# Performance work log

Measured on AMD Instinct MI355X. Metric: run time of the kernel, lower is better.

The kernel has to match this reference:

```python
import jax, jax.numpy as jnp
import numpy as np

N = 100000   # nodes
E = 1000000  # edges
G = 64       # graphs in batch
DIN, DH, DOUT = 128, 128, 64
BN_EPS = 1e-5


def setup_inputs() -> dict:
    key = jax.random.key(0)
    ks = jax.random.split(key, 20)
    inp = {}
    inp['x'] = jax.random.normal(ks[0], (N, DIN), dtype=jnp.float32)
    inp['edge_index'] = jax.random.randint(ks[1], (2, E), 0, N, dtype=jnp.int64)
    inp['batch'] = jnp.sort(jax.random.randint(ks[2], (N,), 0, G, dtype=jnp.int64))
    # GCN conv weights (stored [in, out]) + biases
    s = lambda k, i, o: jax.random.normal(k, (i, o), dtype=jnp.float32) / np.sqrt(i)
    inp['W1'] = s(ks[3], DIN, DH);  inp['b1'] = jnp.zeros((DH,), jnp.float32)
    inp['W2'] = s(ks[4], DH, DH);   inp['b2'] = jnp.zeros((DH,), jnp.float32)
    inp['W3'] = s(ks[5], DH, DOUT); inp['b3'] = jnp.zeros((DOUT,), jnp.float32)
    # BatchNorm params/buffers (eval mode)
    inp['g1'] = jnp.ones((DH,), jnp.float32);  inp['beta1'] = jnp.zeros((DH,), jnp.float32)
    inp['g2'] = jnp.ones((DH,), jnp.float32);  inp['beta2'] = jnp.zeros((DH,), jnp.float32)
    inp['mean1'] = jnp.zeros((DH,), jnp.float32); inp['var1'] = jnp.ones((DH,), jnp.float32)
    inp['mean2'] = jnp.zeros((DH,), jnp.float32); inp['var2'] = jnp.ones((DH,), jnp.float32)
    # GlobalAttention gate_nn: Linear(DOUT,DH) ReLU Linear(DH,1)
    inp['Wg1'] = s(ks[6], DOUT, DH); inp['bg1'] = jnp.zeros((DH,), jnp.float32)
    inp['Wg2'] = s(ks[7], DH, 1);    inp['bg2'] = jnp.zeros((1,), jnp.float32)
    # head MLP: Linear(DOUT,DH) ReLU Linear(DH,DOUT)
    inp['Wm1'] = s(ks[8], DOUT, DH); inp['bm1'] = jnp.zeros((DH,), jnp.float32)
    inp['Wm2'] = s(ks[9], DH, DOUT); inp['bm2'] = jnp.zeros((DOUT,), jnp.float32)
    return inp


def _gcn_conv(x, W, b, src, dst):
    # PyG GCNConv: add self-loops, sym-normalize, linear, scatter-sum, bias
    h = x @ W                                            # [N, out]
    deg = jnp.ones((N,), h.dtype).at[dst].add(1.0)       # in-degree + self-loop
    dinv = jax.lax.rsqrt(deg)
    norm = dinv[src] * dinv[dst]                         # [E]
    msg = h[src] * norm[:, None]                         # gather + scale
    out = jax.ops.segment_sum(msg, dst, num_segments=N)  # scatter
    out = out + h * (dinv * dinv)[:, None]               # self-loop term
    return out + b


def _bn(x, g, beta, mean, var):
    return (x - mean) * jax.lax.rsqrt(var + BN_EPS) * g + beta


def reference(x, edge_index, batch, W1, b1, W2, b2, W3, b3,
              g1, beta1, g2, beta2, mean1, var1, mean2, var2,
              Wg1, bg1, Wg2, bg2, Wm1, bm1, Wm2, bm2):
    src, dst = edge_index[0], edge_index[1]
    h = jax.nn.relu(_bn(_gcn_conv(x, W1, b1, src, dst), g1, beta1, mean1, var1))
    h = jax.nn.relu(_bn(_gcn_conv(h, W2, b2, src, dst), g2, beta2, mean2, var2))
    h = _gcn_conv(h, W3, b3, src, dst)                   # [N, DOUT]
    # GlobalAttention pooling: per-graph softmax of gate scores
    gate = jax.nn.relu(h @ Wg1 + bg1) @ Wg2 + bg2        # [N, 1]
    gate = gate[:, 0]
    m = jax.ops.segment_max(gate, batch, num_segments=G)
    e = jnp.exp(gate - m[batch])
    s = jax.ops.segment_sum(e, batch, num_segments=G)
    a = e / s[batch]                                     # [N]
    pooled = jax.ops.segment_sum(h * a[:, None], batch, num_segments=G)  # [G, DOUT]
    # MLP head (dropout off in eval)
    return jax.nn.relu(pooled @ Wm1 + bm1) @ Wm2 + bm2   # [G, DOUT]
```

## Files before the change

kernel.cpp:

```cpp
#include <hip/hip_runtime.h>
#include <hip/hip_bf16.h>
#include <hip/hip_fp16.h>
#include <math.h>

#define NN 100000
#define EE 1000000
#define GG 64
#define BN_EPS 1e-5f
#define CPB 16
#define EB 4096
#define NBLK ((EE + EB - 1) / EB)
#define NBUCK ((NN + 511) / 512)

typedef __attribute__((ext_vector_type(8))) short bf16x8;
typedef __attribute__((ext_vector_type(4))) float f32x4;

__device__ inline short f2bf(float f) {
  unsigned u = __float_as_uint(f);
  u = u + 0x7fff + ((u >> 16) & 1);
  return (short)(u >> 16);
}
__device__ inline float bf2f(short h) {
  return __uint_as_float(((unsigned)(unsigned short)h) << 16);
}

__device__ inline unsigned fenc(float f) {
  int b = __float_as_int(f);
  return (b < 0) ? ~(unsigned)b : ((unsigned)b | 0x80000000u);
}
__device__ inline float fdec(unsigned u) {
  int b = (u & 0x80000000u) ? (int)(u & 0x7fffffffu) : (int)~u;
  return __int_as_float(b);
}

__device__ inline void acc2(float& a0, float& a1, unsigned u) {
  asm("v_fma_mix_f32 %0, %2, 1.0, %0 op_sel:[0,0,0] op_sel_hi:[1,0,0]\n\t"
      "v_fma_mix_f32 %1, %2, 1.0, %1 op_sel:[1,0,0] op_sel_hi:[1,0,0]"
      : "+v"(a0), "+v"(a1)
      : "v"(u));
}
__device__ inline void acc8(float* a, uint4 u) {
  acc2(a[0], a[1], u.x);
  acc2(a[2], a[3], u.y);
  acc2(a[4], a[5], u.z);
  acc2(a[6], a[7], u.w);
}
__device__ inline uint4 zsel(uint4 u, int ok) {
  uint4 r;
  r.x = ok ? u.x : 0u;
  r.y = ok ? u.y : 0u;
  r.z = ok ? u.z : 0u;
  r.w = ok ? u.w : 0u;
  return r;
}

__global__ __launch_bounds__(256) void k_bhist(const int* __restrict__ dst,
                                               int* __restrict__ bhist, int E) {
  __shared__ int h[256];
  int t = threadIdx.x;
  h[t] = 0;
  __syncthreads();
  int base = blockIdx.x * EB;
#pragma unroll
  for (int j = 0; j < EB / 256; ++j) {
    int i = base + j * 256 + t;
    if (i < E) atomicAdd(&h[dst[i] >> 9], 1);
  }
  __syncthreads();
  bhist[blockIdx.x * 256 + t] = h[t];
}

__global__ __launch_bounds__(256) void k_bscan1(int* __restrict__ bhist,
                                                int* __restrict__ btot) {
  __shared__ int s[256];
  int bin = blockIdx.x, t = threadIdx.x;
  int v = (t < NBLK) ? bhist[t * 256 + bin] : 0;
  s[t] = v;
  __syncthreads();
  for (int o = 1; o < 256; o <<= 1) {
    int u = (t >= o) ? s[t - o] : 0;
    __syncthreads();
    s[t] += u;
    __syncthreads();
  }
  if (t < NBLK) bhist[t * 256 + bin] = s[t] - v;
  if (t == 255) btot[bin] = s[255];
}

__global__ __launch_bounds__(256) void k_bscan2(const int* __restrict__ btot,
                                                int* __restrict__ bstart) {
  __shared__ int s[256];
  int t = threadIdx.x;
  int v = btot[t];
  s[t] = v;
  __syncthreads();
  for (int o = 1; o < 256; o <<= 1) {
    int u = (t >= o) ? s[t - o] : 0;
    __syncthreads();
    s[t] += u;
    __syncthreads();
  }
  bstart[t] = s[t] - v;
}

__global__ __launch_bounds__(256) void k_bscat(const int* __restrict__ src,
                                               const int* __restrict__ dst,
                                               const int* __restrict__ bhist,
                                               const int* __restrict__ bstart,
                                               int2* __restrict__ pairs, int E) {
  __shared__ int h[256];
  __shared__ int base[256];
  int t = threadIdx.x;
  h[t] = 0;
  __syncthreads();
  int b0 = blockIdx.x * EB;
  int ds[EB / 256], rk[EB / 256];
#pragma unroll
  for (int j = 0; j < EB / 256; ++j) {
    int i = b0 + j * 256 + t;
    if (i < E) {
      int d = dst[i];
      ds[j] = d;
      rk[j] = atomicAdd(&h[d >> 9], 1);
    } else
      ds[j] = -1;
  }
  __syncthreads();
  base[t] = bstart[t] + bhist[blockIdx.x * 256 + t];
  __syncthreads();
#pragma unroll
  for (int j = 0; j < EB / 256; ++j) {
    int i = b0 + j * 256 + t;
    if (ds[j] >= 0) {
      int pos = base[ds[j] >> 9] + rk[j];
      pairs[pos] = make_int2(src[i], ds[j]);
    }
  }
}

__global__ __launch_bounds__(256) void k_bfill(const int2* __restrict__ pairs,
                                               const int* __restrict__ bstart,
                                               int* __restrict__ rowstart,
                                               int* __restrict__ eidx,
                                               float* __restrict__ dinv, int N,
                                               int E) {
  __shared__ int h[512];
  __shared__ int ex[512];
  __shared__ int ps[256];
  const int b = blockIdx.x;
  const int n0 = b << 9;
  const int e0 = bstart[b], e1 = bstart[b + 1];
  const int t = threadIdx.x;
  h[t] = 0;
  h[t + 256] = 0;
  __syncthreads();
  for (int i = e0 + t; i < e1; i += 256) atomicAdd(&h[pairs[i].y - n0], 1);
  __syncthreads();
  int v0 = h[2 * t], v1 = h[2 * t + 1];
  int sp = v0 + v1;
  ps[t] = sp;
  __syncthreads();
  for (int o = 1; o < 256; o <<= 1) {
    int u = (t >= o) ? ps[t - o] : 0;
    __syncthreads();
    ps[t] += u;
    __syncthreads();
  }
  int ex0 = ps[t] - sp;
  ex[2 * t] = ex0;
  ex[2 * t + 1] = ex0 + v0;
  __syncthreads();
  for (int i = t; i < 512; i += 256) {
    int node = n0 + i;
    if (node < N) {
      rowstart[node] = e0 + ex[i];
      dinv[node] = rsqrtf(1.0f + (float)h[i]);
    }
  }
  if (b == 0 && t == 0) rowstart[N] = E;
  __syncthreads();
  for (int i = e0 + t; i < e1; i += 256) {
    int2 p = pairs[i];
    int r = atomicAdd(&ex[p.y - n0], 1);
    eidx[e0 + r] = p.x;
  }
}

__global__ __launch_bounds__(256) void k_prep(
    const float* __restrict__ W1, const float* __restrict__ W2,
    const float* __restrict__ W3, const float* __restrict__ Wg1,
    short* __restrict__ wt, const float* __restrict__ g1,
    const float* __restrict__ b1, const float* __restrict__ m1,
    const float* __restrict__ v1, const float* __restrict__ g2,
    const float* __restrict__ b2, const float* __restrict__ m2,
    const float* __restrict__ v2, float* __restrict__ s1,
    float* __restrict__ h1, float* __restrict__ s2, float* __restrict__ h2,
    const int* __restrict__ batch, int* __restrict__ gstart,
    float* __restrict__ pooledw, int N) {
  const int b = blockIdx.x, t = threadIdx.x;
  if (b < 192) {
    int i = b * 256 + t;
    const float* W;
    short *hi, *lo;
    int K, M, idx;
    if (i < 16384) {
      W = W1; hi = wt; lo = wt + 16384; K = 128; M = 128; idx = i;
    } else if (i < 32768) {
      W = W2; hi = wt + 32768; lo = wt + 49152; K = 128; M = 128; idx = i - 16384;
    } else if (i < 40960) {
      W = W3; hi = wt + 65536; lo = wt + 73728; K = 128; M = 64; idx = i - 32768;
    } else {
      W = Wg1; hi = wt + 81920; lo = wt + 90112; K = 64; M = 128; idx = i - 40960;
    }
    int k = idx / M, n = idx % M;
    float w = W[idx];
    short h = f2bf(w);
    hi[n * K + k] = h;
    lo[n * K + k] = f2bf(w - bf2f(h));
  } else if (b == 192) {
    if (t < 128) {
      float s = g1[t] * rsqrtf(v1[t] + BN_EPS);
      s1[t] = s;
      h1[t] = b1[t] - m1[t] * s;
    } else {
      int j = t - 128;
      float s = g2[j] * rsqrtf(v2[j] + BN_EPS);
      s2[j] = s;
      h2[j] = b2[j] - m2[j] * s;
    }
  } else {
    if (t <= GG) {
      int lo = 0, hi = N;
      while (lo < hi) {
        int mid = (lo + hi) >> 1;
        if (batch[mid] < t) lo = mid + 1;
        else hi = mid;
      }
      gstart[t] = lo;
    }
    for (int i = t; i < GG * 64 + GG + GG; i += 256) pooledw[i] = 0.f;
  }
}

template <int K, int M, int CTB>
__global__ __launch_bounds__(256, 3) void k_mgemm1(
    const float* __restrict__ Xf, const short* __restrict__ Wthi,
    const short* __restrict__ Wtlo, const float* __restrict__ dinv,
    __half* __restrict__ Y, int nrows) {
  constexpr int NC = K / 32;
  constexpr int KP = K + 8;
  constexpr int R = 2;
  __shared__ short lds[2 * CTB * 16 * KP];
  const int lane = threadIdx.x & 63;
  const int wave = threadIdx.x >> 6;
  const int m16 = lane & 15;
  const int quad = lane >> 4;
  const int rowbase = blockIdx.x * 128 + wave * 32;
  const int cbase = blockIdx.y * CTB * 16;

  bf16x8 ahi[R][NC], alo[R][NC];
#pragma unroll
  for (int t = 0; t < R; ++t) {
    const int arow = rowbase + t * 16 + m16;
    const bool rok = arow < nrows;
#pragma unroll
    for (int c = 0; c < NC; ++c) {
      const int k0 = c * 32 + quad * 8;
      float4 v0 = make_float4(0.f, 0.f, 0.f, 0.f), v1 = v0;
      if (rok) {
        v0 = *(const float4*)(Xf + (size_t)arow * K + k0);
        v1 = *(const float4*)(Xf + (size_t)arow * K + k0 + 4);
      }
      float vv[8] = {v0.x, v0.y, v0.z, v0.w, v1.x, v1.y, v1.z, v1.w};
#pragma unroll
      for (int j = 0; j < 8; ++j) {
        short h = f2bf(vv[j]);
        ahi[t][c][j] = h;
        alo[t][c][j] = f2bf(vv[j] - bf2f(h));
      }
    }
  }

  {
    constexpr int ELEMS = CTB * 16 * K;
#pragma unroll
    for (int i = threadIdx.x * 8; i < ELEMS; i += 256 * 8) {
      const int r = i / K, c = i % K;
      *(bf16x8*)(&lds[r * KP + c]) =
          *(const bf16x8*)(Wthi + (size_t)(cbase + r) * K + c);
      *(bf16x8*)(&lds[CTB * 16 * KP + r * KP + c]) =
          *(const bf16x8*)(Wtlo + (size_t)(cbase + r) * K + c);
    }
  }

  float dv[R][4];
#pragma unroll
  for (int t = 0; t < R; ++t)
#pragma unroll
    for (int r = 0; r < 4; ++r) {
      int row = rowbase + t * 16 + quad * 4 + r;
      dv[t][r] = (row < nrows) ? dinv[row] : 0.f;
    }

  __syncthreads();

  f32x4 accs[CTB][R];
#pragma unroll
  for (int ct = 0; ct < CTB; ++ct) {
    bf16x8 bhi[NC], blo[NC];
    const int wrow = (ct * 16 + m16) * KP + quad * 8;
#pragma unroll
    for (int c = 0; c < NC; ++c) {
      bhi[c] = *(const bf16x8*)(&lds[wrow + c * 32]);
      blo[c] = *(const bf16x8*)(&lds[CTB * 16 * KP + wrow + c * 32]);
    }
#pragma unroll
    for (int t = 0; t < R; ++t) {
      f32x4 acc = {0.f, 0.f, 0.f, 0.f};
#pragma unroll
      for (int c = 0; c < NC; ++c) {
        acc = __builtin_amdgcn_mfma_f32_16x16x32_bf16(ahi[t][c], bhi[c], acc, 0, 0, 0);
        acc = __builtin_amdgcn_mfma_f32_16x16x32_bf16(ahi[t][c], blo[c], acc, 0, 0, 0);
        acc = __builtin_amdgcn_mfma_f32_16x16x32_bf16(alo[t][c], bhi[c], acc, 0, 0, 0);
      }
      accs[ct][t] = acc;
    }
  }

  constexpr int COLS = CTB * 16;
  constexpr int SP = COLS + 8;
  __syncthreads();
#pragma unroll
  for (int ct = 0; ct < CTB; ++ct)
#pragma unroll
    for (int t = 0; t < R; ++t)
#pragma unroll
      for (int r = 0; r < 4; ++r) {
        const int row_l = wave * 32 + t * 16 + quad * 4 + r;
        float v = accs[ct][t][r] * dv[t][r];
        __half hv = __float2half(v);
        lds[row_l * SP + ct * 16 + m16] = *(short*)&hv;
      }
  __syncthreads();
  constexpr int TOT = 128 * COLS;
#pragma unroll
  for (int p = 0; p < TOT / (256 * 8); ++p) {
    const int idx8 = (p * 256 + threadIdx.x) * 8;
    const int row_l = idx8 / COLS;
    const int col0 = idx8 % COLS;
    const int grow = blockIdx.x * 128 + row_l;
    if (grow < nrows) {
      bf16x8 v = *(const bf16x8*)(&lds[row_l * SP + col0]);
      *(bf16x8*)(Y + (size_t)grow * M + cbase + col0) = v;
    }
  }
}

template <int MOUT>
__global__ __launch_bounds__(512) void k_aggf(
    const __half* __restrict__ hp, const int* __restrict__ rowstart,
    const int* __restrict__ eidx, const float* __restrict__ dinv,
    const float* __restrict__ bias, const float* __restrict__ bns,
    const float* __restrict__ bnh, const short* __restrict__ wthi,
    const short* __restrict__ wtlo, __half* __restrict__ hbout, int N) {
  __shared__ short Ahi[16][136];
  __shared__ short Alo[16][136];
  __shared__ short St[16][MOUT + 8];
  const int lane = threadIdx.x & 63;
  const int wv = threadIdx.x >> 6;
  const int node_l = wv * 2 + (lane >> 5);
  const int slot = (lane >> 4) & 1;
  const int sub = lane & 15;
  const int w = blockIdx.x * 16 + node_l;
  const bool valid = w < N;
  const unsigned subo = (unsigned)sub * 16u;
  const float di = valid ? dinv[w] : 0.f;
  const int lo = valid ? rowstart[w] : 0;
  const int hi = valid ? rowstart[w + 1] : 0;
  const int hi1 = hi - 1;
  const char* hpb = (const char*)hp;
  float a[8] = {0.f, 0.f, 0.f, 0.f, 0.f, 0.f, 0.f, 0.f};

  int e = lo + slot;
  while (e < hi) {
    int idx[8], ss[8];
    uint4 uu[8];
#pragma unroll
    for (int p = 0; p < 8; ++p) {
      idx[p] = e + 2 * p;
      ss[p] = eidx[min(idx[p], hi1)];
    }
#pragma unroll
    for (int p = 0; p < 8; ++p)
      uu[p] = *(const uint4*)(hpb + ((unsigned)ss[p] * 256u + subo));
#pragma unroll
    for (int p = 0; p < 8; ++p) {
      uu[p] = zsel(uu[p], idx[p] < hi);
      acc8(a, uu[p]);
    }
    e += 16;
  }
#pragma unroll
  for (int j = 0; j < 8; ++j) a[j] += __shfl_xor(a[j], 16, 64);

  if (slot == 0) {
    short hs[8], ls[8];
    if (valid) {
      uint4 us = *(const uint4*)(hpb + ((unsigned)w * 256u + subo));
      acc8(a, us);
      float4 b0 = *(const float4*)(bias + sub * 8);
      float4 b1 = *(const float4*)(bias + sub * 8 + 4);
      float r[8];
      r[0] = a[0] * di + b0.x;
      r[1] = a[1] * di + b0.y;
      r[2] = a[2] * di + b0.z;
      r[3] = a[3] * di + b0.w;
      r[4] = a[4] * di + b1.x;
      r[5] = a[5] * di + b1.y;
      r[6] = a[6] * di + b1.z;
      r[7] = a[7] * di + b1.w;
      float4 s0 = *(const float4*)(bns + sub * 8);
      float4 s1 = *(const float4*)(bns + sub * 8 + 4);
      float4 h0 = *(const float4*)(bnh + sub * 8);
      float4 h1 = *(const float4*)(bnh + sub * 8 + 4);
      float sv[8] = {s0.x, s0.y, s0.z, s0.w, s1.x, s1.y, s1.z, s1.w};
      float hv[8] = {h0.x, h0.y, h0.z, h0.w, h1.x, h1.y, h1.z, h1.w};
#pragma unroll
      for (int j = 0; j < 8; ++j) {
        float ev = fmaxf(r[j] * sv[j] + hv[j], 0.f);
        short hb = f2bf(ev);
        float res = ev - bf2f(hb);
        hs[j] = hb;
        ls[j] = (short)(__float_as_uint(res) >> 16);
      }
    } else {
#pragma unroll
      for (int j = 0; j < 8; ++j) {
        hs[j] = 0;
        ls[j] = 0;
      }
    }
#pragma unroll
    for (int j = 0; j < 8; ++j) {
      Ahi[node_l][sub * 8 + j] = hs[j];
      Alo[node_l][sub * 8 + j] = ls[j];
    }
  }
  __syncthreads();

  const int m16 = lane & 15;
  const int quad = lane >> 4;
  constexpr int CT = MOUT / 16;
  if (wv < CT) {
    bf16x8 fah[4], fal[4];
#pragma unroll
    for (int c = 0; c < 4; ++c) {
      fah[c] = *(const bf16x8*)(&Ahi[m16][c * 32 + quad * 8]);
      fal[c] = *(const bf16x8*)(&Alo[m16][c * 32 + quad * 8]);
    }
    bf16x8 bhi[4], blo[4];
    const int wrow = (wv * 16 + m16) * 128 + quad * 8;
#pragma unroll
    for (int c = 0; c < 4; ++c) {
      bhi[c] = *(const bf16x8*)(wthi + wrow + c * 32);
      blo[c] = *(const bf16x8*)(wtlo + wrow + c * 32);
    }
    f32x4 acc = {0.f, 0.f, 0.f, 0.f};
#pragma unroll
    for (int c = 0; c < 4; ++c) {
      acc = __builtin_amdgcn_mfma_f32_16x16x32_bf16(fah[c], bhi[c], acc, 0, 0, 0);
      acc = __builtin_amdgcn_mfma_f32_16x16x32_bf16(fah[c], blo[c], acc, 0, 0, 0);
      acc = __builtin_amdgcn_mfma_f32_16x16x32_bf16(fal[c], bhi[c], acc, 0, 0, 0);
    }
#pragma unroll
    for (int r = 0; r < 4; ++r) {
      const int grow = blockIdx.x * 16 + quad * 4 + r;
      const float dvv = (grow < N) ? dinv[grow] : 0.f;
      __half hv = __float2half(acc[r] * dvv);
      St[quad * 4 + r][wv * 16 + m16] = *(short*)&hv;
    }
  }
  __syncthreads();

  constexpr int SEGS = MOUT / 8;
  const int tid = threadIdx.x;
  if (tid < 16 * SEGS) {
    const int row = tid / SEGS, seg = tid % SEGS;
    const int grow = blockIdx.x * 16 + row;
    if (grow < N)
      *(bf16x8*)(hbout + (size_t)grow * MOUT + seg * 8) =
          *(const bf16x8*)(&St[row][seg * 8]);
  }
}

__global__ __launch_bounds__(256) void k_agg3g(
    const __half* __restrict__ hp, const int* __restrict__ rowstart,
    const int* __restrict__ eidx, const float* __restrict__ dinv,
    const float* __restrict__ bias, const short* __restrict__ wg1hi,
    const short* __restrict__ wg1lo, const float* __restrict__ bg1,
    const float* __restrict__ Wg2v, const float* __restrict__ bg2v,
    float* __restrict__ outf, float* __restrict__ gate, int N) {
  __shared__ short Ahi[16][72];
  __shared__ short Alo[16][72];
  const int lane = threadIdx.x & 63;
  const int wv = threadIdx.x >> 6;
  const int grp = lane >> 4;
  const int slot = (lane >> 3) & 1;
  const int sub = lane & 7;
  const int node_l = wv * 4 + grp;
  const int w = blockIdx.x * 16 + node_l;
  const bool valid = w < N;

  for (int i = threadIdx.x; i < 16 * 72; i += 256) {
    (&Ahi[0][0])[i] = 0;
    (&Alo[0][0])[i] = 0;
  }
  __syncthreads();

  const unsigned subo = (unsigned)sub * 16u;
  const float di = valid ? dinv[w] : 0.f;
  const int lo = valid ? rowstart[w] : 0;
  const int hi = valid ? rowstart[w + 1] : 0;
  const int hi1 = hi - 1;
  const char* hpb = (const char*)hp;
  float a[8] = {0.f, 0.f, 0.f, 0.f, 0.f, 0.f, 0.f, 0.f};

  int e = lo + slot;
  while (e < hi) {
    int idx[8], ss[8];
    uint4 uu[8];
#pragma unroll
    for (int p = 0; p < 8; ++p) {
      idx[p] = e + 2 * p;
      ss[p] = eidx[min(idx[p], hi1)];
    }
#pragma unroll
    for (int p = 0; p < 8; ++p)
      uu[p] = *(const uint4*)(hpb + ((unsigned)ss[p] * 128u + subo));
#pragma unroll
    for (int p = 0; p < 8; ++p) {
      uu[p] = zsel(uu[p], idx[p] < hi);
      acc8(a, uu[p]);
    }
    e += 16;
  }
#pragma unroll
  for (int j = 0; j < 8; ++j) a[j] += __shfl_xor(a[j], 8, 64);

  if (slot == 0 && valid) {
    uint4 us = *(const uint4*)(hpb + ((unsigned)w * 128u + subo));
    acc8(a, us);
    float4 b0 = *(const float4*)(bias + sub * 8);
    float4 b1 = *(const float4*)(bias + sub * 8 + 4);
    float r[8];
    r[0] = a[0] * di + b0.x;
    r[1] = a[1] * di + b0.y;
    r[2] = a[2] * di + b0.z;
    r[3] = a[3] * di + b0.w;
    r[4] = a[4] * di + b1.x;
    r[5] = a[5] * di + b1.y;
    r[6] = a[6] * di + b1.z;
    r[7] = a[7] * di + b1.w;
    *(float4*)(outf + (size_t)w * 64 + sub * 8) =
        make_float4(r[0], r[1], r[2], r[3]);
    *(float4*)(outf + (size_t)w * 64 + sub * 8 + 4) =
        make_float4(r[4], r[5], r[6], r[7]);
#pragma unroll
    for (int j = 0; j < 8; ++j) {
      short h = f2bf(r[j]);
      Ahi[node_l][sub * 8 + j] = h;
      Alo[node_l][sub * 8 + j] = f2bf(r[j] - bf2f(h));
    }
  }
  __syncthreads();

  if (wv != 0) return;
  const int m16 = lane & 15;
  const int quad = lane >> 4;
  bf16x8 fa_hi[2], fa_lo[2];
#pragma unroll
  for (int c = 0; c < 2; ++c) {
    fa_hi[c] = *(const bf16x8*)(&Ahi[m16][c * 32 + quad * 8]);
    fa_lo[c] = *(const bf16x8*)(&Alo[m16][c * 32 + quad * 8]);
  }
  float gp[4] = {0.f, 0.f, 0.f, 0.f};
#pragma unroll
  for (int ct = 0; ct < 8; ++ct) {
    bf16x8 bhi[2], blo[2];
    const int wrow = (ct * 16 + m16) * 64 + quad * 8;
#pragma unroll
    for (int c = 0; c < 2; ++c) {
      bhi[c] = *(const bf16x8*)(wg1hi + wrow + c * 32);
      blo[c] = *(const bf16x8*)(wg1lo + wrow + c * 32);
    }
    f32x4 acc = {0.f, 0.f, 0.f, 0.f};
#pragma unroll
    for (int c = 0; c < 2; ++c) {
      acc = __builtin_amdgcn_mfma_f32_16x16x32_bf16(fa_hi[c], bhi[c], acc, 0, 0, 0);
      acc = __builtin_amdgcn_mfma_f32_16x16x32_bf16(fa_hi[c], blo[c], acc, 0, 0, 0);
      acc = __builtin_amdgcn_mfma_f32_16x16x32_bf16(fa_lo[c], bhi[c], acc, 0, 0, 0);
    }
    const int col = ct * 16 + m16;
    const float gb = bg1[col], wg = Wg2v[col];
#pragma unroll
    for (int r = 0; r < 4; ++r) gp[r] += fmaxf(acc[r] + gb, 0.f) * wg;
  }
#pragma unroll
  for (int o = 1; o < 16; o <<= 1)
#pragma unroll
    for (int r = 0; r < 4; ++r) gp[r] += __shfl_xor(gp[r], o, 64);
  if (m16 == 0) {
    const float b2 = bg2v[0];
#pragma unroll
    for (int r = 0; r < 4; ++r) {
      const int node = blockIdx.x * 16 + quad * 4 + r;
      if (node < N) gate[node] = gp[r] + b2;
    }
  }
}

__global__ __launch_bounds__(256) void k_pmax(const float* __restrict__ gate,
                                              const int* __restrict__ gstart,
                                              unsigned* __restrict__ gmaxu) {
  __shared__ unsigned red[256];
  const int g = blockIdx.x / CPB;
  const int c = blockIdx.x % CPB;
  const int lo = gstart[g], hi = gstart[g + 1];
  const int len = hi - lo;
  const int b0 = lo + (int)(((long long)len * c) / CPB);
  const int b1 = lo + (int)(((long long)len * (c + 1)) / CPB);
  unsigned mx = 0u;
  for (int i = b0 + threadIdx.x; i < b1; i += 256) mx = max(mx, fenc(gate[i]));
  red[threadIdx.x] = mx;
  __syncthreads();
  for (int o = 128; o; o >>= 1) {
    if (threadIdx.x < o)
      red[threadIdx.x] = max(red[threadIdx.x], red[threadIdx.x + o]);
    __syncthreads();
  }
  if (threadIdx.x == 0 && red[0] != 0u) atomicMax(&gmaxu[g], red[0]);
}

__global__ __launch_bounds__(256) void k_psum(const float* __restrict__ gate,
                                              const float* __restrict__ h3,
                                              const unsigned* __restrict__ gmaxu,
                                              const int* __restrict__ gstart,
                                              float* __restrict__ pooledw,
                                              float* __restrict__ ssum) {
  __shared__ float accs[4][64];
  __shared__ float ses[4];
  const int g = blockIdx.x / CPB;
  const int c = blockIdx.x % CPB;
  const int lo = gstart[g], hi = gstart[g + 1];
  const int len = hi - lo;
  const int b0 = lo + (int)(((long long)len * c) / CPB);
  const int b1 = lo + (int)(((long long)len * (c + 1)) / CPB);
  const int wave = threadIdx.x >> 6, lane = threadIdx.x & 63;
  const float m = fdec(gmaxu[g]);
  float acc = 0.f, se = 0.f;
  for (int i = b0 + wave; i < b1; i += 4) {
    float e = expf(gate[i] - m);
    acc += e * h3[(size_t)i * 64 + lane];
    se += e;
  }
  accs[wave][lane] = acc;
  if (lane == 0) ses[wave] = se;
  __syncthreads();
  if (threadIdx.x < 64) {
    float a = accs[0][threadIdx.x] + accs[1][threadIdx.x] +
              accs[2][threadIdx.x] + accs[3][threadIdx.x];
    if (a != 0.f) atomicAdd(&pooledw[g * 64 + threadIdx.x], a);
  }
  if (threadIdx.x == 64) {
    float s = ses[0] + ses[1] + ses[2] + ses[3];
    if (s != 0.f) atomicAdd(&ssum[g], s);
  }
}

__global__ __launch_bounds__(256) void k_head(const float* __restrict__ pooledw,
                                              const float* __restrict__ ssum,
                                              const float* __restrict__ Wm1,
                                              const float* __restrict__ bm1,
                                              const float* __restrict__ Wm2,
                                              const float* __restrict__ bm2,
                                              float* __restrict__ out) {
  __shared__ float P[64 * 64];
  __shared__ float T[64 * 128];
  int tid = threadIdx.x;
  for (int i = tid; i < 4096; i += 256) {
    float s = ssum[i >> 6];
    P[i] = pooledw[i] * ((s > 0.f) ? 1.0f / s : 0.f);
  }
  __syncthreads();
  for (int e = tid; e < 8192; e += 256) {
    int r = e >> 7, c = e & 127;
    float a = bm1[c];
    for (int k = 0; k < 64; ++k) a += P[r * 64 + k] * Wm1[k * 128 + c];
    T[e] = fmaxf(a, 0.f);
  }
  __syncthreads();
  for (int e = tid; e < 4096; e += 256) {
    int r = e >> 6, c = e & 63;
    float a = bm2[c];
    for (int k = 0; k < 128; ++k) a += T[r * 128 + k] * Wm2[k * 64 + c];
    out[e] = a;
  }
}

extern "C" void kernel_launch(void* const* d_in, const int* in_sizes, int n_in,
                              void* d_out, int out_size, void* d_ws,
                              size_t ws_size, hipStream_t stream) {
  const int N = NN, E = EE;
  const float* x = (const float*)d_in[0];
  const int* ei = (const int*)d_in[1];
  const int* batch = (const int*)d_in[2];
  const float* W1 = (const float*)d_in[3];
  const float* b1 = (const float*)d_in[4];
  const float* W2 = (const float*)d_in[5];
  const float* b2 = (const float*)d_in[6];
  const float* W3 = (const float*)d_in[7];
  const float* b3 = (const float*)d_in[8];
  const float* g1 = (const float*)d_in[9];
  const float* beta1 = (const float*)d_in[10];
  const float* g2 = (const float*)d_in[11];
  const float* beta2 = (const float*)d_in[12];
  const float* mean1 = (const float*)d_in[13];
  const float* var1 = (const float*)d_in[14];
  const float* mean2 = (const float*)d_in[15];
  const float* var2 = (const float*)d_in[16];
  const float* Wg1 = (const float*)d_in[17];
  const float* bg1 = (const float*)d_in[18];
  const float* Wg2 = (const float*)d_in[19];
  const float* bg2 = (const float*)d_in[20];
  const float* Wm1 = (const float*)d_in[21];
  const float* bm1 = (const float*)d_in[22];
  const float* Wm2 = (const float*)d_in[23];
  const float* bm2 = (const float*)d_in[24];
  float* out = (float*)d_out;

  const int* src = ei;
  const int* dst = ei + E;

  char* wsb = (char*)d_ws;
  size_t off = 0;
  auto alloc = [&](size_t elems) -> void* {
    void* p = wsb + off;
    off += elems * 4;
    return p;
  };
  int* rowstart = (int*)alloc(N + 4);
  int* eidx = (int*)alloc(E);
  int2* pairs = (int2*)alloc((size_t)E * 2);
  int* bhist = (int*)alloc(NBLK * 256 + 256);
  int* btot = (int*)alloc(256);
  int* bstart = (int*)alloc(256);
  float* dinv = (float*)alloc(N);
  float* gate = (float*)alloc(N);
  __half* hbufA = (__half*)alloc((size_t)N * 64);
  __half* hbufB = (__half*)alloc((size_t)N * 64);
  float* fbuf = (float*)alloc((size_t)N * 64);
  short* wt = (short*)alloc(49152);
  float* bn1s = (float*)alloc(128);
  float* bn1h = (float*)alloc(128);
  float* bn2s = (float*)alloc(128);
  float* bn2h = (float*)alloc(128);
  float* pooledw = (float*)alloc(GG * 64);
  float* ssum = (float*)alloc(GG);
  unsigned* gmaxu = (unsigned*)alloc(GG);
  int* gstart = (int*)alloc(GG + 4);
  (void)ws_size;
  (void)n_in;
  (void)in_sizes;
  (void)out_size;

  k_bhist<<<NBLK, 256, 0, stream>>>(dst, bhist, E);
  k_bscan1<<<256, 256, 0, stream>>>(bhist, btot);
  k_bscan2<<<1, 256, 0, stream>>>(btot, bstart);
  k_bscat<<<NBLK, 256, 0, stream>>>(src, dst, bhist, bstart, pairs, E);
  k_bfill<<<NBUCK, 256, 0, stream>>>(pairs, bstart, rowstart, eidx, dinv, N, E);

  k_prep<<<194, 256, 0, stream>>>(W1, W2, W3, Wg1, wt, g1, beta1, mean1, var1,
                                  g2, beta2, mean2, var2, bn1s, bn1h, bn2s,
                                  bn2h, batch, gstart, pooledw, N);

  const int gbb = (N + 127) / 128;
  const int ab16 = (N + 15) / 16;

  k_mgemm1<128, 128, 4><<<dim3(gbb, 2), 256, 0, stream>>>(x, wt, wt + 16384,
                                                          dinv, hbufA, N);
  k_aggf<128><<<ab16, 512, 0, stream>>>(hbufA, rowstart, eidx, dinv, b1, bn1s,
                                        bn1h, wt + 32768, wt + 49152, hbufB,
                                        N);
  k_aggf<64><<<ab16, 512, 0, stream>>>(hbufB, rowstart, eidx, dinv, b2, bn2s,
                                       bn2h, wt + 65536, wt + 73728, hbufA, N);
  k_agg3g<<<ab16, 256, 0, stream>>>(hbufA, rowstart, eidx, dinv, b3,
                                    wt + 81920, wt + 90112, bg1, Wg2, bg2,
                                    fbuf, gate, N);

  k_pmax<<<GG * CPB, 256, 0, stream>>>(gate, gstart, gmaxu);
  k_psum<<<GG * CPB, 256, 0, stream>>>(gate, fbuf, gmaxu, gstart, pooledw,
                                       ssum);

  k_head<<<1, 256, 0, stream>>>(pooledw, ssum, Wm1, bm1, Wm2, bm2, out);
}
```

Measured before the change: 457.0 us.

## Merge prep into histogram kernel, fuse pooling into one per-graph kernel, vectorize LDS stores

```diff
diff --git a/kernel.cpp b/kernel.cpp
--- a/kernel.cpp
+++ b/kernel.cpp
@@ -7,7 +7,6 @@
 #define EE 1000000
 #define GG 64
 #define BN_EPS 1e-5f
-#define CPB 16
 #define EB 4096
 #define NBLK ((EE + EB - 1) / EB)
 #define NBUCK ((NN + 511) / 512)
@@ -22,15 +21,6 @@
 }
 __device__ inline float bf2f(short h) {
   return __uint_as_float(((unsigned)(unsigned short)h) << 16);
-}
-
-__device__ inline unsigned fenc(float f) {
-  int b = __float_as_int(f);
-  return (b < 0) ? ~(unsigned)b : ((unsigned)b | 0x80000000u);
-}
-__device__ inline float fdec(unsigned u) {
-  int b = (u & 0x80000000u) ? (int)(u & 0x7fffffffu) : (int)~u;
-  return __int_as_float(b);
 }
 
 __device__ inline void acc2(float& a0, float& a1, unsigned u) {
@@ -54,20 +44,74 @@
   return r;
 }
 
-__global__ __launch_bounds__(256) void k_bhist(const int* __restrict__ dst,
-                                               int* __restrict__ bhist, int E) {
-  __shared__ int h[256];
-  int t = threadIdx.x;
-  h[t] = 0;
-  __syncthreads();
-  int base = blockIdx.x * EB;
-#pragma unroll
-  for (int j = 0; j < EB / 256; ++j) {
-    int i = base + j * 256 + t;
-    if (i < E) atomicAdd(&h[dst[i] >> 9], 1);
-  }
-  __syncthreads();
-  bhist[blockIdx.x * 256 + t] = h[t];
+__global__ __launch_bounds__(256) void k_bhist_prep(
+    const int* __restrict__ dst, int* __restrict__ bhist, int E,
+    const float* __restrict__ W1, const float* __restrict__ W2,
+    const float* __restrict__ W3, const float* __restrict__ Wg1,
+    short* __restrict__ wt, const float* __restrict__ g1,
+    const float* __restrict__ b1, const float* __restrict__ m1,
+    const float* __restrict__ v1, const float* __restrict__ g2,
+    const float* __restrict__ b2, const float* __restrict__ m2,
+    const float* __restrict__ v2, float* __restrict__ s1,
+    float* __restrict__ h1, float* __restrict__ s2, float* __restrict__ h2,
+    const int* __restrict__ batch, int* __restrict__ gstart, int N) {
+  const int t = threadIdx.x;
+  if (blockIdx.x < NBLK) {
+    __shared__ int h[256];
+    h[t] = 0;
+    __syncthreads();
+    int base = blockIdx.x * EB;
+#pragma unroll
+    for (int j = 0; j < EB / 256; ++j) {
+      int i = base + j * 256 + t;
+      if (i < E) atomicAdd(&h[dst[i] >> 9], 1);
+    }
+    __syncthreads();
+    bhist[blockIdx.x * 256 + t] = h[t];
+    return;
+  }
+  const int b = blockIdx.x - NBLK;
+  if (b < 192) {
+    int i = b * 256 + t;
+    const float* W;
+    short *hi, *lo;
+    int K, M, idx;
+    if (i < 16384) {
+      W = W1; hi = wt; lo = wt + 16384; K = 128; M = 128; idx = i;
+    } else if (i < 32768) {
+      W = W2; hi = wt + 32768; lo = wt + 49152; K = 128; M = 128; idx = i - 16384;
+    } else if (i < 40960) {
+      W = W3; hi = wt + 65536; lo = wt + 73728; K = 128; M = 64; idx = i - 32768;
+    } else {
+      W = Wg1; hi = wt + 81920; lo = wt + 90112; K = 64; M = 128; idx = i - 40960;
+    }
+    int k = idx / M, n = idx % M;
+    float w = W[idx];
+    short h = f2bf(w);
+    hi[n * K + k] = h;
+    lo[n * K + k] = f2bf(w - bf2f(h));
+  } else if (b == 192) {
+    if (t < 128) {
+      float s = g1[t] * rsqrtf(v1[t] + BN_EPS);
+      s1[t] = s;
+      h1[t] = b1[t] - m1[t] * s;
+    } else {
+      int j = t - 128;
+      float s = g2[j] * rsqrtf(v2[j] + BN_EPS);
+      s2[j] = s;
+      h2[j] = b2[j] - m2[j] * s;
+    }
+  } else {
+    if (t <= GG) {
+      int lo = 0, hi = N;
+      while (lo < hi) {
+        int mid = (lo + hi) >> 1;
+        if (batch[mid] < t) lo = mid + 1;
+        else hi = mid;
+      }
+      gstart[t] = lo;
+    }
+  }
 }
 
 __global__ __launch_bounds__(256) void k_bscan1(int* __restrict__ bhist,
@@ -183,62 +227,6 @@
     int2 p = pairs[i];
     int r = atomicAdd(&ex[p.y - n0], 1);
     eidx[e0 + r] = p.x;
-  }
-}
-
-__global__ __launch_bounds__(256) void k_prep(
-    const float* __restrict__ W1, const float* __restrict__ W2,
-    const float* __restrict__ W3, const float* __restrict__ Wg1,
-    short* __restrict__ wt, const float* __restrict__ g1,
-    const float* __restrict__ b1, const float* __restrict__ m1,
-    const float* __restrict__ v1, const float* __restrict__ g2,
-    const float* __restrict__ b2, const float* __restrict__ m2,
-    const float* __restrict__ v2, float* __restrict__ s1,
-    float* __restrict__ h1, float* __restrict__ s2, float* __restrict__ h2,
-    const int* __restrict__ batch, int* __restrict__ gstart,
-    float* __restrict__ pooledw, int N) {
-  const int b = blockIdx.x, t = threadIdx.x;
-  if (b < 192) {
-    int i = b * 256 + t;
-    const float* W;
-    short *hi, *lo;
-    int K, M, idx;
-    if (i < 16384) {
-      W = W1; hi = wt; lo = wt + 16384; K = 128; M = 128; idx = i;
-    } else if (i < 32768) {
-      W = W2; hi = wt + 32768; lo = wt + 49152; K = 128; M = 128; idx = i - 16384;
-    } else if (i < 40960) {
-      W = W3; hi = wt + 65536; lo = wt + 73728; K = 128; M = 64; idx = i - 32768;
-    } else {
-      W = Wg1; hi = wt + 81920; lo = wt + 90112; K = 64; M = 128; idx = i - 40960;
-    }
-    int k = idx / M, n = idx % M;
-    float w = W[idx];
-    short h = f2bf(w);
-    hi[n * K + k] = h;
-    lo[n * K + k] = f2bf(w - bf2f(h));
-  } else if (b == 192) {
-    if (t < 128) {
-      float s = g1[t] * rsqrtf(v1[t] + BN_EPS);
-      s1[t] = s;
-      h1[t] = b1[t] - m1[t] * s;
-    } else {
-      int j = t - 128;
-      float s = g2[j] * rsqrtf(v2[j] + BN_EPS);
-      s2[j] = s;
-      h2[j] = b2[j] - m2[j] * s;
-    }
-  } else {
-    if (t <= GG) {
-      int lo = 0, hi = N;
-      while (lo < hi) {
-        int mid = (lo + hi) >> 1;
-        if (batch[mid] < t) lo = mid + 1;
-        else hi = mid;
-      }
-      gstart[t] = lo;
-    }
-    for (int i = t; i < GG * 64 + GG + GG; i += 256) pooledw[i] = 0.f;
   }
 }
 
@@ -404,7 +392,8 @@
   for (int j = 0; j < 8; ++j) a[j] += __shfl_xor(a[j], 16, 64);
 
   if (slot == 0) {
-    short hs[8], ls[8];
+    bf16x8 hv8 = bf16x8{0, 0, 0, 0, 0, 0, 0, 0};
+    bf16x8 lv8 = bf16x8{0, 0, 0, 0, 0, 0, 0, 0};
     if (valid) {
       uint4 us = *(const uint4*)(hpb + ((unsigned)w * 256u + subo));
       acc8(a, us);
@@ -430,21 +419,12 @@
         float ev = fmaxf(r[j] * sv[j] + hv[j], 0.f);
         short hb = f2bf(ev);
         float res = ev - bf2f(hb);
-        hs[j] = hb;
-        ls[j] = (short)(__float_as_uint(res) >> 16);
+        hv8[j] = hb;
+        lv8[j] = (short)(__float_as_uint(res) >> 16);
       }
-    } else {
-#pragma unroll
-      for (int j = 0; j < 8; ++j) {
-        hs[j] = 0;
-        ls[j] = 0;
-      }
-    }
-#pragma unroll
-    for (int j = 0; j < 8; ++j) {
-      Ahi[node_l][sub * 8 + j] = hs[j];
-      Alo[node_l][sub * 8 + j] = ls[j];
-    }
+    }
+    *(bf16x8*)(&Ahi[node_l][sub * 8]) = hv8;
+    *(bf16x8*)(&Alo[node_l][sub * 8]) = lv8;
   }
   __syncthreads();
 
@@ -565,12 +545,15 @@
         make_float4(r[0], r[1], r[2], r[3]);
     *(float4*)(outf + (size_t)w * 64 + sub * 8 + 4) =
         make_float4(r[4], r[5], r[6], r[7]);
+    bf16x8 hv8, lv8;
 #pragma unroll
     for (int j = 0; j < 8; ++j) {
       short h = f2bf(r[j]);
-      Ahi[node_l][sub * 8 + j] = h;
-      Alo[node_l][sub * 8 + j] = f2bf(r[j] - bf2f(h));
-    }
+      hv8[j] = h;
+      lv8[j] = f2bf(r[j] - bf2f(h));
+    }
+    *(bf16x8*)(&Ahi[node_l][sub * 8]) = hv8;
+    *(bf16x8*)(&Alo[node_l][sub * 8]) = lv8;
   }
   __syncthreads();
 
@@ -619,66 +602,47 @@
   }
 }
 
-__global__ __launch_bounds__(256) void k_pmax(const float* __restrict__ gate,
+__global__ __launch_bounds__(512) void k_pool(const float* __restrict__ gate,
+                                              const float* __restrict__ h3,
                                               const int* __restrict__ gstart,
-                                              unsigned* __restrict__ gmaxu) {
-  __shared__ unsigned red[256];
-  const int g = blockIdx.x / CPB;
-  const int c = blockIdx.x % CPB;
+                                              float* __restrict__ pooledw) {
+  __shared__ float red[512];
+  __shared__ float accs[8][64];
+  __shared__ float ses[8];
+  const int g = blockIdx.x;
   const int lo = gstart[g], hi = gstart[g + 1];
-  const int len = hi - lo;
-  const int b0 = lo + (int)(((long long)len * c) / CPB);
-  const int b1 = lo + (int)(((long long)len * (c + 1)) / CPB);
-  unsigned mx = 0u;
-  for (int i = b0 + threadIdx.x; i < b1; i += 256) mx = max(mx, fenc(gate[i]));
-  red[threadIdx.x] = mx;
-  __syncthreads();
-  for (int o = 128; o; o >>= 1) {
-    if (threadIdx.x < o)
-      red[threadIdx.x] = max(red[threadIdx.x], red[threadIdx.x + o]);
-    __syncthreads();
-  }
-  if (threadIdx.x == 0 && red[0] != 0u) atomicMax(&gmaxu[g], red[0]);
-}
-
-__global__ __launch_bounds__(256) void k_psum(const float* __restrict__ gate,
-                                              const float* __restrict__ h3,
-                                              const unsigned* __restrict__ gmaxu,
-                                              const int* __restrict__ gstart,
-                                              float* __restrict__ pooledw,
-                                              float* __restrict__ ssum) {
-  __shared__ float accs[4][64];
-  __shared__ float ses[4];
-  const int g = blockIdx.x / CPB;
-  const int c = blockIdx.x % CPB;
-  const int lo = gstart[g], hi = gstart[g + 1];
-  const int len = hi - lo;
-  const int b0 = lo + (int)(((long long)len * c) / CPB);
-  const int b1 = lo + (int)(((long long)len * (c + 1)) / CPB);
-  const int wave = threadIdx.x >> 6, lane = threadIdx.x & 63;
-  const float m = fdec(gmaxu[g]);
+  const int tid = threadIdx.x;
+  float mx = -INFINITY;
+  for (int i = lo + tid; i < hi; i += 512) mx = fmaxf(mx, gate[i]);
+  red[tid] = mx;
+  __syncthreads();
+  for (int o = 256; o; o >>= 1) {
+    if (tid < o) red[tid] = fmaxf(red[tid], red[tid + o]);
+    __syncthreads();
+  }
+  const float m = red[0];
+  const int wv = tid >> 6, lane = tid & 63;
   float acc = 0.f, se = 0.f;
-  for (int i = b0 + wave; i < b1; i += 4) {
+  for (int i = lo + wv; i < hi; i += 8) {
     float e = expf(gate[i] - m);
     acc += e * h3[(size_t)i * 64 + lane];
     se += e;
   }
-  accs[wave][lane] = acc;
-  if (lane == 0) ses[wave] = se;
-  __syncthreads();
-  if (threadIdx.x < 64) {
-    float a = accs[0][threadIdx.x] + accs[1][threadIdx.x] +
-              accs[2][threadIdx.x] + accs[3][threadIdx.x];
-    if (a != 0.f) atomicAdd(&pooledw[g * 64 + threadIdx.x], a);
-  }
-  if (threadIdx.x == 64) {
-    float s = ses[0] + ses[1] + ses[2] + ses[3];
-    if (s != 0.f) atomicAdd(&ssum[g], s);
+  accs[wv][lane] = acc;
+  if (lane == 0) ses[wv] = se;
+  __syncthreads();
+  if (tid < 64) {
+    float a = 0.f, s = 0.f;
+#pragma unroll
+    for (int k = 0; k < 8; ++k) {
+      a += accs[k][tid];
+      s += ses[k];
+    }
+    pooledw[g * 64 + tid] = (s > 0.f) ? a / s : 0.f;
   }
 }
 
 __global__ __launch_bounds__(256) void k_head(const float* __restrict__ pooledw,
-                                              const float* __restrict__ ssum,
                                               const float* __restrict__ Wm1,
                                               const float* __restrict__ bm1,
                                               const float* __restrict__ Wm2,
@@ -687,10 +651,7 @@
   __shared__ float P[64 * 64];
   __shared__ float T[64 * 128];
   int tid = threadIdx.x;
-  for (int i = tid; i < 4096; i += 256) {
-    float s = ssum[i >> 6];
-    P[i] = pooledw[i] * ((s > 0.f) ? 1.0f / s : 0.f);
-  }
+  for (int i = tid; i < 4096; i += 256) P[i] = pooledw[i];
   __syncthreads();
   for (int e = tid; e < 8192; e += 256) {
     int r = e >> 7, c = e & 127;
@@ -765,23 +726,19 @@
   float* bn2s = (float*)alloc(128);
   float* bn2h = (float*)alloc(128);
   float* pooledw = (float*)alloc(GG * 64);
-  float* ssum = (float*)alloc(GG);
-  unsigned* gmaxu = (unsigned*)alloc(GG);
   int* gstart = (int*)alloc(GG + 4);
   (void)ws_size;
   (void)n_in;
   (void)in_sizes;
   (void)out_size;
 
-  k_bhist<<<NBLK, 256, 0, stream>>>(dst, bhist, E);
+  k_bhist_prep<<<NBLK + 194, 256, 0, stream>>>(
+      dst, bhist, E, W1, W2, W3, Wg1, wt, g1, beta1, mean1, var1, g2, beta2,
+      mean2, var2, bn1s, bn1h, bn2s, bn2h, batch, gstart, N);
   k_bscan1<<<256, 256, 0, stream>>>(bhist, btot);
   k_bscan2<<<1, 256, 0, stream>>>(btot, bstart);
   k_bscat<<<NBLK, 256, 0, stream>>>(src, dst, bhist, bstart, pairs, E);
   k_bfill<<<NBUCK, 256, 0, stream>>>(pairs, bstart, rowstart, eidx, dinv, N, E);
-
-  k_prep<<<194, 256, 0, stream>>>(W1, W2, W3, Wg1, wt, g1, beta1, mean1, var1,
-                                  g2, beta2, mean2, var2, bn1s, bn1h, bn2s,
-                                  bn2h, batch, gstart, pooledw, N);
 
   const int gbb = (N + 127) / 128;
   const int ab16 = (N + 15) / 16;
@@ -797,9 +754,7 @@
                                     wt + 81920, wt + 90112, bg1, Wg2, bg2,
                                     fbuf, gate, N);
 
-  k_pmax<<<GG * CPB, 256, 0, stream>>>(gate, gstart, gmaxu);
-  k_psum<<<GG * CPB, 256, 0, stream>>>(gate, fbuf, gmaxu, gstart, pooledw,
-                                       ssum);
-
-  k_head<<<1, 256, 0, stream>>>(pooledw, ssum, Wm1, bm1, Wm2, bm2, out);
-}
+  k_pool<<<GG, 512, 0, stream>>>(gate, fbuf, gstart, pooledw);
+
+  k_head<<<1, 256, 0, stream>>>(pooledw, Wm1, bm1, Wm2, bm2, out);
+}
```

Result: slower. 500.8 us (+9.6%).
